# Optimization experiments

Measured on AMD Instinct MI355X. Metric: run time of the kernel, lower is better.

## Reference

```python
import jax, jax.numpy as jnp
import numpy as np

NUM_RING = 16
MAX_RING = 1520
EPS = 1e-5


def setup_inputs() -> dict:
    key = jax.random.key(0)
    B, C, N = 16, 64, 16384
    cnt = N // NUM_RING  # 1024 points per ring, sorted
    k1, k2, k3, k4, k5 = jax.random.split(key, 5)
    x = jax.random.normal(k1, (B, C, N), dtype=jnp.float32)
    # ring ids: sorted, exactly cnt points per ring (the module assumes sorted,
    # identical-count rings across batch)
    ring = jnp.broadcast_to(jnp.arange(N, dtype=jnp.int64) // cnt, (B, N))
    # random-upsample indices: concat(arange(cnt), randperm(cnt)[:MAX_RING-cnt])
    rng = np.random.default_rng(0)
    up = MAX_RING - cnt  # 496
    choice = np.empty((B, NUM_RING, MAX_RING), dtype=np.int64)
    for b in range(B):
        for r in range(NUM_RING):
            choice[b, r, :cnt] = np.arange(cnt)
            choice[b, r, cnt:] = rng.permutation(cnt)[:up]
    choice = jnp.asarray(choice)
    # grouped Conv1d(64 -> 128, kernel 1, groups=16): weight [128, 4, 1] -> [16, 8, 4]
    Wg = jax.random.normal(k2, (NUM_RING, 8, 4), dtype=jnp.float32) * 0.5
    bias = jax.random.normal(k3, (128,), dtype=jnp.float32) * 0.1
    gamma = jnp.ones((128,), dtype=jnp.float32)
    beta = jnp.zeros((128,), dtype=jnp.float32)
    return {"x": x, "Wg": Wg, "bias": bias, "gamma": gamma, "beta": beta,
            "ring": ring, "choice": choice}


def reference(x, Wg, bias, gamma, beta, ring, choice):
    B, C, N = x.shape  # C = 64
    R, MR = NUM_RING, MAX_RING
    cnt = N // R
    L = R * MR  # 24320

    xt = jnp.transpose(x, (0, 2, 1))  # [B, N, 64]
    # per-ring gather with random upsample to MAX_RING points
    idx = (jnp.arange(R, dtype=choice.dtype)[None, :, None] * cnt + choice)  # [B,R,MR]
    gathered = jnp.take_along_axis(xt, idx.reshape(B, L, 1), axis=1)  # [B, L, 64]

    # faithful to torch: cat(...).view(B, 64, -1) is a raw reshape (channel-scrambling)
    xc = gathered.reshape(B, C, L)  # [B, 64, L]

    # grouped 1x1 conv: 16 groups, 4 in / 8 out channels each
    xg = xc.reshape(B, R, 4, L)
    y = jnp.einsum('goc,bgcl->bgol', Wg, xg).reshape(B, 128, L)
    y = y + bias[None, :, None]

    # BatchNorm1d (training mode: batch statistics, biased variance)
    mean = jnp.mean(y, axis=(0, 2))
    var = jnp.var(y, axis=(0, 2))
    y = gamma[None, :, None] * (y - mean[None, :, None]) * jax.lax.rsqrt(var + EPS)[None, :, None] + beta[None, :, None]

    # per-ring max over MAX_RING slots, broadcast back to original ring sizes
    pooled = jnp.max(y.reshape(B, 128, R, MR), axis=-1)  # [B, 128, R]
    out = jnp.repeat(pooled, cnt, axis=2)  # [B, 128, N]
    return out
```

## Files before the change

kernel.cpp:

```cpp
#include <hip/hip_runtime.h>
#include <float.h>

#define NB    16
#define CIN   64
#define NPT   16384
#define NRING 16
#define MAXR  1520
#define CNT   1024
#define LTOT  (NRING*MAXR)
#define MBLK  380
#define NCH   128
#define NBLK1 (NB*CIN*2)
#define IDXS  500

typedef float fx4 __attribute__((ext_vector_type(4)));

__device__ __forceinline__ float sload(float v) {
    return __int_as_float(__builtin_amdgcn_readfirstlane(__float_as_int(v)));
}

__global__ __launch_bounds__(512) void k1_gather_conv(
    const float* __restrict__ x, const float* __restrict__ Wg,
    const float* __restrict__ bias, const float* __restrict__ gamma,
    const int* __restrict__ choice,
    float* __restrict__ p_sum, float* __restrict__ p_sqs,
    float* __restrict__ p_max)
{
    __shared__ float xs[8192];
    __shared__ unsigned short ilds[8*IDXS];

    const int blk = blockIdx.x;
    const int b  = blk >> 7;
    const int cp = (blk >> 1) & 63;
    const int h  = blk & 1;
    const int t  = threadIdx.x;

    {
        const float4* src = (const float4*)(x + ((size_t)(b*CIN + cp)) * NPT + h*8192);
        float4* dst = (float4*)xs;
        #pragma unroll
        for (int i = 0; i < 4; ++i) {
            const int J  = t + i*512;
            const int gg = J >> 8;
            const int j  = J & 255;
            dst[(gg << 8) + ((j + gg) & 255)] = src[J];
        }
    }
    {
        #pragma unroll
        for (int i = 0; i < 2; ++i) {
            const int J  = t + i*512;
            const int gg = J >> 7;
            const int j  = J & 127;
            if (j < 124) {
                const int4 v = *(const int4*)(choice + ((size_t)(b*NRING + h*8 + gg))*MAXR + 1024 + j*4);
                ushort4 u;
                u.x = (unsigned short)v.x; u.y = (unsigned short)v.y;
                u.z = (unsigned short)v.z; u.w = (unsigned short)v.w;
                *(ushort4*)(ilds + gg*IDXS + j*4) = u;
            }
        }
    }
    __syncthreads();

    const int g8   = t >> 6;
    const int lane = t & 63;
    const int r    = lane >> 2;
    const int s    = lane & 3;
    const int g    = h*8 + g8;

    float w[8][4], bs[8];
    #pragma unroll
    for (int o = 0; o < 8; ++o) {
        const int ch = g*8 + o;
        const float sg = (gamma[ch] < 0.0f) ? -1.0f : 1.0f;
        bs[o] = sload(sg * bias[ch]);
        #pragma unroll
        for (int c = 0; c < 4; ++c) w[o][c] = sload(sg * Wg[ch*4 + c]);
    }

    int mlo = (r*MAXR - cp + 63) >> 6;
    int mhi = ((r+1)*MAXR - cp + 63) >> 6;
    if (mhi > MBLK) mhi = MBLK;

    float smax[8], ssum[8], ssq[8];
    #pragma unroll
    for (int o = 0; o < 8; ++o) { smax[o] = -FLT_MAX; ssum[o] = 0.f; ssq[o] = 0.f; }

    const int rot = g8 << 2;
    const float* __restrict__ xg = xs + (g8 << 10);
    const unsigned short* __restrict__ ig = ilds + g8*IDXS;

    for (int m = mlo + s; m < mhi; m += 4) {
        const int off2  = (m >= 264) ? (m - 264) : 0;
        const int lidx2 = ig[off2];
        const int idx2  = (m < 264) ? (760 + m) : lidx2;
        const int idx3  = ig[116 + m];
        const float v0 = xg[( m        + rot) & 1023];
        const float v1 = xg[((380 + m) + rot) & 1023];
        const float v2 = xg[( idx2     + rot) & 1023];
        const float v3 = xg[( idx3     + rot) & 1023];
        #pragma unroll
        for (int o = 0; o < 8; ++o) {
            float y = fmaf(w[o][0], v0, fmaf(w[o][1], v1,
                      fmaf(w[o][2], v2, fmaf(w[o][3], v3, bs[o]))));
            smax[o] = fmaxf(smax[o], y);
            ssum[o] += y;
            ssq[o]  = fmaf(y, y, ssq[o]);
        }
    }

    #pragma unroll
    for (int o = 0; o < 8; ++o) {
        smax[o] = fmaxf(smax[o], __shfl_xor(smax[o], 1));
        ssum[o] += __shfl_xor(ssum[o], 1);
        ssq[o]  += __shfl_xor(ssq[o], 1);
        smax[o] = fmaxf(smax[o], __shfl_xor(smax[o], 2));
        ssum[o] += __shfl_xor(ssum[o], 2);
        ssq[o]  += __shfl_xor(ssq[o], 2);
    }

    if (s == 0) {
        float* base = p_max + (((size_t)(b*64 + cp))*NRING + r)*NCH + h*64 + g8*8;
        ((float4*)base)[0] = make_float4(smax[0], smax[1], smax[2], smax[3]);
        ((float4*)base)[1] = make_float4(smax[4], smax[5], smax[6], smax[7]);
    }

    __syncthreads();
    float* redS = xs;
    float* redQ = xs + 1100;
    if (s == 0) {
        #pragma unroll
        for (int o = 0; o < 8; ++o) {
            redS[(g8*8+o)*17 + r] = ssum[o];
            redQ[(g8*8+o)*17 + r] = ssq[o];
        }
    }
    __syncthreads();
    if (t < 64) {
        float S = 0.f, Q = 0.f;
        #pragma unroll
        for (int rr = 0; rr < 16; ++rr) {
            S += redS[t*17 + rr];
            Q += redQ[t*17 + rr];
        }
        const float sg = (gamma[h*64 + t] < 0.0f) ? -1.0f : 1.0f;
        p_sum[(size_t)blk*64 + t] = sg * S;
        p_sqs[(size_t)blk*64 + t] = Q;
    }
}

__global__ __launch_bounds__(256) void k2a_stats(
    const float* __restrict__ p_sum, const float* __restrict__ p_sqs,
    float2* __restrict__ stats)
{
    __shared__ float lsum[256], lsq[256];
    const int ch = blockIdx.x;
    const int hh = ch >> 6, c64 = ch & 63;
    float S = 0.f, Q = 0.f;
    for (int j = threadIdx.x; j < 1024; j += 256) {
        S += p_sum[(size_t)j*128 + hh*64 + c64];
        Q += p_sqs[(size_t)j*128 + hh*64 + c64];
    }
    lsum[threadIdx.x] = S; lsq[threadIdx.x] = Q;
    __syncthreads();
    for (int sred = 128; sred > 0; sred >>= 1) {
        if (threadIdx.x < sred) {
            lsum[threadIdx.x] += lsum[threadIdx.x + sred];
            lsq[threadIdx.x]  += lsq[threadIdx.x + sred];
        }
        __syncthreads();
    }
    if (threadIdx.x == 0) {
        const float inv = 1.0f / (float)((size_t)NB * LTOT);
        float mean = lsum[0] * inv;
        float var  = lsq[0] * inv - mean*mean;
        stats[ch] = make_float2(mean, rsqrtf(var + 1e-5f));
    }
}

__global__ __launch_bounds__(256) void k23_pool_bcast(
    const float* __restrict__ p_max, const float2* __restrict__ stats,
    const float* __restrict__ gamma, const float* __restrict__ beta,
    fx4* __restrict__ out)
{
    __shared__ float part[16][17];
    __shared__ float pool[16];
    const int bc = blockIdx.x;
    const int b  = bc >> 7;
    const int ch = bc & 127;
    const int t  = threadIdx.x;
    const int r  = t >> 4;
    const int ck = t & 15;

    float v = -FLT_MAX;
    #pragma unroll
    for (int k = 0; k < 4; ++k) {
        const int cpi = ck*4 + k;
        v = fmaxf(v, p_max[(((size_t)(b*64 + cpi))*NRING + r)*NCH + ch]);
    }
    part[r][ck] = v;
    __syncthreads();
    if (t < 16) {
        float acc = part[t][0];
        #pragma unroll
        for (int k = 1; k < 16; ++k) acc = fmaxf(acc, part[t][k]);
        const float gm = gamma[ch];
        const float raw = (gm >= 0.0f) ? acc : -acc;
        const float2 st = stats[ch];
        pool[t] = gm * (raw - st.x) * st.y + beta[ch];
    }
    __syncthreads();

    fx4* __restrict__ dst = out + (size_t)bc * (NPT/4);
    #pragma unroll
    for (int i = 0; i < 16; ++i) {
        const int idx = t + i*256;
        const float vv = pool[idx >> 8];
        fx4 val; val.x = vv; val.y = vv; val.z = vv; val.w = vv;
        __builtin_nontemporal_store(val, &dst[idx]);
    }
}

extern "C" void kernel_launch(void* const* d_in, const int* in_sizes, int n_in,
                              void* d_out, int out_size, void* d_ws, size_t ws_size,
                              hipStream_t stream)
{
    const float* x     = (const float*)d_in[0];
    const float* Wg    = (const float*)d_in[1];
    const float* bias  = (const float*)d_in[2];
    const float* gamma = (const float*)d_in[3];
    const float* beta  = (const float*)d_in[4];
    const int* choice  = (const int*)d_in[6];

    float* p_sum = (float*)d_ws;
    float* p_sqs = p_sum + (size_t)2048*64;
    float* p_max = p_sqs + (size_t)2048*64;
    float2* stats = (float2*)(p_max + (size_t)1024*NRING*NCH);

    k1_gather_conv<<<NBLK1, 512, 0, stream>>>(x, Wg, bias, gamma, choice,
                                              p_sum, p_sqs, p_max);
    k2a_stats<<<NCH, 256, 0, stream>>>(p_sum, p_sqs, stats);
    k23_pool_bcast<<<NB*NCH, 256, 0, stream>>>(p_max, stats, gamma, beta, (fx4*)d_out);
}
```

Baseline: 64.58 us.

## Fuse BN stats reduction into pool kernel, drop LDS rotation, unroll gather loop

Removes the separate stats kernel: every pool/broadcast block now redundantly reduces the 1024 partial sums and squares for its channel with wave shuffles, which saves a launch and a dependency at the cost of duplicated reads. The k1 x-load no longer applies the bank-conflict rotation, so LDS reads index the buffer directly. The inner gather/conv loop is fully unrolled into 5 fixed iterations plus a guarded tail, with index loads hoisted ahead of the data loads. Dropping the rotation may bring back LDS bank conflicts across wave groups.

Measured after the change: 63.54 us. Within noise of the previous version (-1.6%).

```diff
diff --git a/kernel.cpp b/kernel.cpp
--- a/kernel.cpp
+++ b/kernel.cpp
@@ -6,7 +6,6 @@
 #define NPT   16384
 #define NRING 16
 #define MAXR  1520
-#define CNT   1024
 #define LTOT  (NRING*MAXR)
 #define MBLK  380
 #define NCH   128
@@ -39,12 +38,7 @@
         const float4* src = (const float4*)(x + ((size_t)(b*CIN + cp)) * NPT + h*8192);
         float4* dst = (float4*)xs;
         #pragma unroll
-        for (int i = 0; i < 4; ++i) {
-            const int J  = t + i*512;
-            const int gg = J >> 8;
-            const int j  = J & 255;
-            dst[(gg << 8) + ((j + gg) & 255)] = src[J];
-        }
+        for (int i = 0; i < 4; ++i) dst[t + i*512] = src[t + i*512];
     }
     {
         #pragma unroll
@@ -79,27 +73,35 @@
         for (int c = 0; c < 4; ++c) w[o][c] = sload(sg * Wg[ch*4 + c]);
     }
 
-    int mlo = (r*MAXR - cp + 63) >> 6;
+    const int mlo = (r*MAXR - cp + 63) >> 6;
     int mhi = ((r+1)*MAXR - cp + 63) >> 6;
     if (mhi > MBLK) mhi = MBLK;
 
-    float smax[8], ssum[8], ssq[8];
-    #pragma unroll
-    for (int o = 0; o < 8; ++o) { smax[o] = -FLT_MAX; ssum[o] = 0.f; ssq[o] = 0.f; }
-
-    const int rot = g8 << 2;
     const float* __restrict__ xg = xs + (g8 << 10);
     const unsigned short* __restrict__ ig = ilds + g8*IDXS;
 
-    for (int m = mlo + s; m < mhi; m += 4) {
-        const int off2  = (m >= 264) ? (m - 264) : 0;
-        const int lidx2 = ig[off2];
-        const int idx2  = (m < 264) ? (760 + m) : lidx2;
-        const int idx3  = ig[116 + m];
-        const float v0 = xg[( m        + rot) & 1023];
-        const float v1 = xg[((380 + m) + rot) & 1023];
-        const float v2 = xg[( idx2     + rot) & 1023];
-        const float v3 = xg[( idx3     + rot) & 1023];
+    float smax[8], ssum[8], ssq[8];
+    #pragma unroll
+    for (int o = 0; o < 8; ++o) { smax[o] = -FLT_MAX; ssum[o] = 0.f; ssq[o] = 0.f; }
+
+    const int m0 = mlo + s;
+
+    int ix2[5], ix3[5];
+    #pragma unroll
+    for (int k = 0; k < 5; ++k) {
+        const int m = m0 + 4*k;
+        const int off2 = (m >= 264) ? (m - 264) : 0;
+        const int l2 = ig[off2];
+        ix2[k] = (m < 264) ? (760 + m) : l2;
+        ix3[k] = ig[116 + m];
+    }
+    #pragma unroll
+    for (int k = 0; k < 5; ++k) {
+        const int m = m0 + 4*k;
+        const float v0 = xg[m];
+        const float v1 = xg[380 + m];
+        const float v2 = xg[ix2[k]];
+        const float v3 = xg[ix3[k]];
         #pragma unroll
         for (int o = 0; o < 8; ++o) {
             float y = fmaf(w[o][0], v0, fmaf(w[o][1], v1,
@@ -107,6 +109,27 @@
             smax[o] = fmaxf(smax[o], y);
             ssum[o] += y;
             ssq[o]  = fmaf(y, y, ssq[o]);
+        }
+    }
+    {
+        const int m = m0 + 20;
+        if (m < mhi) {
+            const int off2 = (m >= 264) ? (m - 264) : 0;
+            const int l2 = ig[off2];
+            const int idx2 = (m < 264) ? (760 + m) : l2;
+            const int idx3 = ig[116 + m];
+            const float v0 = xg[m];
+            const float v1 = xg[380 + m];
+            const float v2 = xg[idx2];
+            const float v3 = xg[idx3];
+            #pragma unroll
+            for (int o = 0; o < 8; ++o) {
+                float y = fmaf(w[o][0], v0, fmaf(w[o][1], v1,
+                          fmaf(w[o][2], v2, fmaf(w[o][3], v3, bs[o]))));
+                smax[o] = fmaxf(smax[o], y);
+                ssum[o] += y;
+                ssq[o]  = fmaf(y, y, ssq[o]);
+            }
         }
     }
 
@@ -150,65 +173,60 @@
     }
 }
 
-__global__ __launch_bounds__(256) void k2a_stats(
+__global__ __launch_bounds__(256) void k23_pool_bcast(
     const float* __restrict__ p_sum, const float* __restrict__ p_sqs,
-    float2* __restrict__ stats)
-{
-    __shared__ float lsum[256], lsq[256];
-    const int ch = blockIdx.x;
-    const int hh = ch >> 6, c64 = ch & 63;
-    float S = 0.f, Q = 0.f;
-    for (int j = threadIdx.x; j < 1024; j += 256) {
-        S += p_sum[(size_t)j*128 + hh*64 + c64];
-        Q += p_sqs[(size_t)j*128 + hh*64 + c64];
-    }
-    lsum[threadIdx.x] = S; lsq[threadIdx.x] = Q;
-    __syncthreads();
-    for (int sred = 128; sred > 0; sred >>= 1) {
-        if (threadIdx.x < sred) {
-            lsum[threadIdx.x] += lsum[threadIdx.x + sred];
-            lsq[threadIdx.x]  += lsq[threadIdx.x + sred];
-        }
-        __syncthreads();
-    }
-    if (threadIdx.x == 0) {
-        const float inv = 1.0f / (float)((size_t)NB * LTOT);
-        float mean = lsum[0] * inv;
-        float var  = lsq[0] * inv - mean*mean;
-        stats[ch] = make_float2(mean, rsqrtf(var + 1e-5f));
-    }
-}
-
-__global__ __launch_bounds__(256) void k23_pool_bcast(
-    const float* __restrict__ p_max, const float2* __restrict__ stats,
+    const float* __restrict__ p_max,
     const float* __restrict__ gamma, const float* __restrict__ beta,
     fx4* __restrict__ out)
 {
     __shared__ float part[16][17];
+    __shared__ float wsum[4], wsq[4];
     __shared__ float pool[16];
     const int bc = blockIdx.x;
     const int b  = bc >> 7;
     const int ch = bc & 127;
     const int t  = threadIdx.x;
-    const int r  = t >> 4;
-    const int ck = t & 15;
-
+    const int hh = ch >> 6, c64 = ch & 63;
+
+    const int r = t >> 4, ck = t & 15;
     float v = -FLT_MAX;
     #pragma unroll
     for (int k = 0; k < 4; ++k) {
         const int cpi = ck*4 + k;
         v = fmaxf(v, p_max[(((size_t)(b*64 + cpi))*NRING + r)*NCH + ch]);
     }
+
+    float S = 0.f, Q = 0.f;
+    #pragma unroll
+    for (int i = 0; i < 4; ++i) {
+        const int jj = t + i*256;
+        const int b2 = jj >> 6, cp2 = jj & 63;
+        const int kb = b2*128 + cp2*2 + hh;
+        S += p_sum[(size_t)kb*64 + c64];
+        Q += p_sqs[(size_t)kb*64 + c64];
+    }
+    #pragma unroll
+    for (int off = 1; off < 64; off <<= 1) {
+        S += __shfl_xor(S, off);
+        Q += __shfl_xor(Q, off);
+    }
     part[r][ck] = v;
-    __syncthreads();
+    if ((t & 63) == 0) { wsum[t >> 6] = S; wsq[t >> 6] = Q; }
+    __syncthreads();
+
     if (t < 16) {
+        const float inv = 1.0f / (float)((size_t)NB * LTOT);
+        const float Sa = wsum[0] + wsum[1] + wsum[2] + wsum[3];
+        const float Qa = wsq[0] + wsq[1] + wsq[2] + wsq[3];
+        const float mean = Sa * inv;
+        const float var  = Qa * inv - mean*mean;
+        const float istd = rsqrtf(var + 1e-5f);
         float acc = part[t][0];
         #pragma unroll
         for (int k = 1; k < 16; ++k) acc = fmaxf(acc, part[t][k]);
         const float gm = gamma[ch];
         const float raw = (gm >= 0.0f) ? acc : -acc;
-        const float2 st = stats[ch];
-        pool[t] = gm * (raw - st.x) * st.y + beta[ch];
+        pool[t] = gm * (raw - mean) * istd + beta[ch];
     }
     __syncthreads();
 
@@ -236,10 +254,9 @@
     float* p_sum = (float*)d_ws;
     float* p_sqs = p_sum + (size_t)2048*64;
     float* p_max = p_sqs + (size_t)2048*64;
-    float2* stats = (float2*)(p_max + (size_t)1024*NRING*NCH);
 
     k1_gather_conv<<<NBLK1, 512, 0, stream>>>(x, Wg, bias, gamma, choice,
                                               p_sum, p_sqs, p_max);
-    k2a_stats<<<NCH, 256, 0, stream>>>(p_sum, p_sqs, stats);
-    k23_pool_bcast<<<NB*NCH, 256, 0, stream>>>(p_max, stats, gamma, beta, (fx4*)d_out);
-}
+    k23_pool_bcast<<<NB*NCH, 256, 0, stream>>>(p_sum, p_sqs, p_max,
+                                               gamma, beta, (fx4*)d_out);
+}
```
